# Optimization experiments

Hardware: AMD Instinct MI355X
Metric: run time of the kernel (lower is better)

## Reference

```python
import jax, jax.numpy as jnp
import numpy as np

H = 64  # hidden_dim
D = 16  # input_dim


def _gru_scan(x, w_ih, w_hh, b_ih, b_hh):
    """Single-direction GRU (PyTorch gate order r,z,n).
    x: [B,T,D] -> ys: [T,B,H] (hidden at each step), h_last: [B,H]."""
    B = x.shape[0]
    # precompute input-to-gate projections for all timesteps: [T,B,3H]
    xg = jnp.einsum('btd,gd->tbg', x, w_ih) + b_ih
    h0 = jnp.zeros((B, w_hh.shape[1]), dtype=x.dtype)

    def step(h, xg_t):
        hg = h @ w_hh.T + b_hh                      # [B,3H]
        xr, xz, xn = jnp.split(xg_t, 3, axis=-1)
        hr, hz, hn = jnp.split(hg, 3, axis=-1)
        r = jax.nn.sigmoid(xr + hr)
        z = jax.nn.sigmoid(xz + hz)
        n = jnp.tanh(xn + r * hn)
        h_new = (1.0 - z) * n + z * h
        return h_new, h_new

    h_last, ys = jax.lax.scan(step, h0, xg)
    return ys, h_last


def setup_inputs() -> dict:
    key = jax.random.key(0)
    ks = jax.random.split(key, 11)
    B, T = 512, 512
    s_i = 1.0 / np.sqrt(H)
    x = jax.random.normal(ks[0], (B, T, D), dtype=jnp.float32)
    def u(k, shape):
        return jax.random.uniform(k, shape, dtype=jnp.float32, minval=-s_i, maxval=s_i)
    return {
        'x': x,
        'w_ih_f': u(ks[1], (3 * H, D)), 'w_hh_f': u(ks[2], (3 * H, H)),
        'b_ih_f': u(ks[3], (3 * H,)),  'b_hh_f': u(ks[4], (3 * H,)),
        'w_ih_b': u(ks[5], (3 * H, D)), 'w_hh_b': u(ks[6], (3 * H, H)),
        'b_ih_b': u(ks[7], (3 * H,)),  'b_hh_b': u(ks[8], (3 * H,)),
        'fc_w': u(ks[9], (1, 2 * H)),  'fc_b': u(ks[10], (1,)),
    }


def reference(x, w_ih_f, w_hh_f, b_ih_f, b_hh_f,
              w_ih_b, w_hh_b, b_ih_b, b_hh_b, fc_w, fc_b):
    # forward direction: output at t=T-1 is the final carry
    _, h_fwd_last = _gru_scan(x, w_ih_f, w_hh_f, b_ih_f, b_hh_f)
    # backward direction: runs over reversed time; its output at original
    # t=T-1 is the FIRST step of the reversed scan
    ys_b, _ = _gru_scan(x[:, ::-1, :], w_ih_b, w_hh_b, b_ih_b, b_hh_b)
    h_bwd_at_last = ys_b[0]                          # [B,H]
    out_last = jnp.concatenate([h_fwd_last, h_bwd_at_last], axis=-1)  # [B,2H]
    y = out_last @ fc_w.T + fc_b                     # [B,1]
    return jnp.squeeze(y, axis=-1)                   # [B]
```

## Files before the change

### kernel.cpp

```cpp
#include <hip/hip_runtime.h>


#define Hh 64
#define Dd 16
#define Tt 512
#define Bb 512
#define CH 32
#define NC (Tt / CH)
#define PLANE (CH * Hh)
#define BUFSZ (3 * PLANE)

typedef float v2f __attribute__((ext_vector_type(2)));

__device__ __forceinline__ float rcp_fast(float v) { return __builtin_amdgcn_rcpf(v); }
__device__ __forceinline__ float sigmoid_fast(float v) {
    return rcp_fast(1.0f + __expf(-v));
}
__device__ __forceinline__ float tanh_fast(float v) {
    return 1.0f - 2.0f * rcp_fast(__expf(2.0f * v) + 1.0f);
}
__device__ __forceinline__ float dot4(float4 a, float4 b) {
    return a.x * b.x + a.y * b.y + a.z * b.z + a.w * b.w;
}
__device__ __forceinline__ void pkfma(v2f& a, v2f b, v2f c) {
    asm("v_pk_fma_f32 %0, %1, %2, %0" : "+v"(a) : "v"(b), "v"(c));
}
__device__ __forceinline__ void lds_barrier() {
    asm volatile("s_waitcnt lgkmcnt(0)\n\ts_barrier" ::: "memory");
}

#define QPK(Q, QI)                                                           \
    {                                                                        \
        const v2f lo_ = { Q.x, Q.y };                                        \
        const v2f hi_ = { Q.z, Q.w };                                        \
        pkfma(ar0, wr2[2*(QI)],     lo_);                                    \
        pkfma(az0, wz2[2*(QI)],     lo_);                                    \
        pkfma(an0, wn2[2*(QI)],     lo_);                                    \
        pkfma(ar1, wr2[2*(QI) + 1], hi_);                                    \
        pkfma(az1, wz2[2*(QI) + 1], hi_);                                    \
        pkfma(an1, wn2[2*(QI) + 1], hi_);                                    \
    }

__global__ __launch_bounds__(256, 2)
void bigru_pc_kernel(const float* __restrict__ x,
                     const float* __restrict__ w_ih_f, const float* __restrict__ w_hh_f,
                     const float* __restrict__ b_ih_f, const float* __restrict__ b_hh_f,
                     const float* __restrict__ w_ih_b, const float* __restrict__ w_hh_b,
                     const float* __restrict__ b_ih_b, const float* __restrict__ b_hh_b,
                     const float* __restrict__ fc_w,  const float* __restrict__ fc_b,
                     float* __restrict__ out)
{
    const int tid  = threadIdx.x;
    const int j    = tid & 63;
    const int w    = tid >> 6;
    const int b    = blockIdx.x;
    const int cons = b & 3;

    __shared__ __align__(16) float xgs[2 * BUFSZ];
    __shared__ __align__(16) float hbuf[Hh];

    const float* xrow = x + (size_t)b * Tt * Dd;

    if (w == cons) {
        v2f wr2[Hh/2], wz2[Hh/2], wn2[Hh/2];
        {
            const float4* r0 = (const float4*)(w_hh_f + (size_t)j            * Hh);
            const float4* r1 = (const float4*)(w_hh_f + (size_t)(Hh + j)     * Hh);
            const float4* r2 = (const float4*)(w_hh_f + (size_t)(2 * Hh + j) * Hh);
#pragma unroll
            for (int q = 0; q < Hh / 4; ++q) {
                float4 a = r0[q]; wr2[2*q] = (v2f){a.x, a.y}; wr2[2*q+1] = (v2f){a.z, a.w};
                float4 c = r1[q]; wz2[2*q] = (v2f){c.x, c.y}; wz2[2*q+1] = (v2f){c.z, c.w};
                float4 e = r2[q]; wn2[2*q] = (v2f){e.x, e.y}; wn2[2*q+1] = (v2f){e.z, e.w};
            }
        }
        const float bhnr = b_hh_f[2 * Hh + j];
        float h = 0.0f;

        for (int c = 0; c < NC; ++c) {
            lds_barrier();
            const float* base = xgs + (c & 1) * BUFSZ + j;
            float par = base[0];
            float paz = base[PLANE];
            float pan = base[2 * PLANE];
#pragma unroll 2
            for (int t = 0; t < CH; ++t) {
                hbuf[j] = h;
                const float4* hq = (const float4*)hbuf;
                float4 q0 = hq[0],  q1 = hq[1],  q2 = hq[2],  q3 = hq[3];
                float4 q4 = hq[4],  q5 = hq[5],  q6 = hq[6],  q7 = hq[7];
                const int tn = (t + 1) & (CH - 1);
                const float* p = base + tn * Hh;
                const float nar = p[0];
                const float naz = p[PLANE];
                const float nan = p[2 * PLANE];

                v2f ar0 = {0.f, 0.f}, ar1 = {0.f, 0.f};
                v2f az0 = {0.f, 0.f}, az1 = {0.f, 0.f};
                v2f an0 = {0.f, 0.f}, an1 = {0.f, 0.f};

                QPK(q0, 0)  QPK(q1, 1)  QPK(q2, 2)  QPK(q3, 3)
                q0 = hq[8];  q1 = hq[9];  q2 = hq[10]; q3 = hq[11];
                QPK(q4, 4)  QPK(q5, 5)  QPK(q6, 6)  QPK(q7, 7)
                q4 = hq[12]; q5 = hq[13]; q6 = hq[14]; q7 = hq[15];
                QPK(q0, 8)  QPK(q1, 9)  QPK(q2, 10) QPK(q3, 11)
                QPK(q4, 12) QPK(q5, 13) QPK(q6, 14) QPK(q7, 15)

                const float sr = (ar0.x + ar0.y) + (ar1.x + ar1.y);
                const float sz = (az0.x + az0.y) + (az1.x + az1.y);
                const float sn = (an0.x + an0.y) + (an1.x + an1.y);

                const float r = sigmoid_fast(par + sr);
                const float z = sigmoid_fast(paz + sz);
                const float n = tanh_fast(pan + r * (bhnr + sn));
                h = n + z * (h - n);
                par = nar; paz = naz; pan = nan;
            }
        }

        float ar   = b_ih_b[j]          + b_hh_b[j];
        float az   = b_ih_b[Hh + j]     + b_hh_b[Hh + j];
        float axn  = b_ih_b[2 * Hh + j];
        const float bhnb = b_hh_b[2 * Hh + j];
        {
            const float4* xl = (const float4*)(xrow + (size_t)(Tt - 1) * Dd);
            float4 xv0 = xl[0], xv1 = xl[1], xv2 = xl[2], xv3 = xl[3];
            const float4* q0 = (const float4*)(w_ih_b + (size_t)j            * Dd);
            const float4* q1 = (const float4*)(w_ih_b + (size_t)(Hh + j)     * Dd);
            const float4* q2 = (const float4*)(w_ih_b + (size_t)(2 * Hh + j) * Dd);
            ar  += dot4(q0[0], xv0) + dot4(q0[1], xv1) + dot4(q0[2], xv2) + dot4(q0[3], xv3);
            az  += dot4(q1[0], xv0) + dot4(q1[1], xv1) + dot4(q1[2], xv2) + dot4(q1[3], xv3);
            axn += dot4(q2[0], xv0) + dot4(q2[1], xv1) + dot4(q2[2], xv2) + dot4(q2[3], xv3);
        }
        const float rb = sigmoid_fast(ar);
        const float zb = sigmoid_fast(az);
        const float nb = tanh_fast(axn + rb * bhnb);
        const float hb = (1.0f - zb) * nb;

        float v = fc_w[j] * h + fc_w[Hh + j] * hb;
#pragma unroll
        for (int off = 32; off > 0; off >>= 1)
            v += __shfl_xor(v, off, 64);
        if (j == 0) out[b] = v + fc_b[0];
    } else {
        const int pw = (w > cons) ? (w - 1) : w;
        float4 wir[4], wiz[4], win[4];
        {
            const float4* p0 = (const float4*)(w_ih_f + (size_t)j            * Dd);
            const float4* p1 = (const float4*)(w_ih_f + (size_t)(Hh + j)     * Dd);
            const float4* p2 = (const float4*)(w_ih_f + (size_t)(2 * Hh + j) * Dd);
#pragma unroll
            for (int q = 0; q < 4; ++q) { wir[q] = p0[q]; wiz[q] = p1[q]; win[q] = p2[q]; }
        }
        const float bxr = b_ih_f[j]          + b_hh_f[j];
        const float bxz = b_ih_f[Hh + j]     + b_hh_f[Hh + j];
        const float bxn = b_ih_f[2 * Hh + j];

#define PRODUCE(C1) {                                                        \
            float* obase = xgs + ((C1) & 1) * BUFSZ + j;                     \
            for (int tt = pw; tt < CH; tt += 3) {                            \
                const float4* xq = (const float4*)(xrow + (size_t)((C1) * CH + tt) * Dd); \
                float4 x0 = xq[0], x1 = xq[1], x2 = xq[2], x3 = xq[3];       \
                float ar_ = bxr + dot4(wir[0],x0) + dot4(wir[1],x1)          \
                                + dot4(wir[2],x2) + dot4(wir[3],x3);         \
                float az_ = bxz + dot4(wiz[0],x0) + dot4(wiz[1],x1)          \
                                + dot4(wiz[2],x2) + dot4(wiz[3],x3);         \
                float an_ = bxn + dot4(win[0],x0) + dot4(win[1],x1)          \
                                + dot4(win[2],x2) + dot4(win[3],x3);         \
                float* o = obase + tt * Hh;                                  \
                o[0] = ar_; o[PLANE] = az_; o[2 * PLANE] = an_;              \
            }                                                                \
        }

        PRODUCE(0);
        for (int c = 0; c < NC; ++c) {
            lds_barrier();
            if (c + 1 < NC) PRODUCE(c + 1);
        }
#undef PRODUCE
    }
}

extern "C" void kernel_launch(void* const* d_in, const int* in_sizes, int n_in,
                              void* d_out, int out_size, void* d_ws, size_t ws_size,
                              hipStream_t stream) {
    const float* x      = (const float*)d_in[0];
    const float* w_ih_f = (const float*)d_in[1];
    const float* w_hh_f = (const float*)d_in[2];
    const float* b_ih_f = (const float*)d_in[3];
    const float* b_hh_f = (const float*)d_in[4];
    const float* w_ih_b = (const float*)d_in[5];
    const float* w_hh_b = (const float*)d_in[6];
    const float* b_ih_b = (const float*)d_in[7];
    const float* b_hh_b = (const float*)d_in[8];
    const float* fc_w   = (const float*)d_in[9];
    const float* fc_b   = (const float*)d_in[10];

    bigru_pc_kernel<<<dim3(Bb), dim3(256), 0, stream>>>(
        x, w_ih_f, w_hh_f, b_ih_f, b_hh_f,
        w_ih_b, w_hh_b, b_ih_b, b_hh_b, fc_w, fc_b,
        (float*)d_out);
}
```

Measured before the change: 287.2 us.

## Process two batch rows per block to interleave independent GRU recurrences

```diff
diff --git a/kernel.cpp b/kernel.cpp
--- a/kernel.cpp
+++ b/kernel.cpp
@@ -5,10 +5,12 @@
 #define Dd 16
 #define Tt 512
 #define Bb 512
-#define CH 32
+#define NBLK (Bb / 2)
+#define CH 16
 #define NC (Tt / CH)
 #define PLANE (CH * Hh)
-#define BUFSZ (3 * PLANE)
+#define BATCHSZ (3 * PLANE)
+#define BUFSZ (2 * BATCHSZ)
 
 typedef float v2f __attribute__((ext_vector_type(2)));
 
@@ -29,37 +31,42 @@
     asm volatile("s_waitcnt lgkmcnt(0)\n\ts_barrier" ::: "memory");
 }
 
-#define QPK(Q, QI)                                                           \
+#define PAIRQ(QI, QA, QB)                                                    \
     {                                                                        \
-        const v2f lo_ = { Q.x, Q.y };                                        \
-        const v2f hi_ = { Q.z, Q.w };                                        \
-        pkfma(ar0, wr2[2*(QI)],     lo_);                                    \
-        pkfma(az0, wz2[2*(QI)],     lo_);                                    \
-        pkfma(an0, wn2[2*(QI)],     lo_);                                    \
-        pkfma(ar1, wr2[2*(QI) + 1], hi_);                                    \
-        pkfma(az1, wz2[2*(QI) + 1], hi_);                                    \
-        pkfma(an1, wn2[2*(QI) + 1], hi_);                                    \
+        const v2f la_ = { QA.x, QA.y }, ha_ = { QA.z, QA.w };                \
+        const v2f lb_ = { QB.x, QB.y }, hb_ = { QB.z, QB.w };                \
+        pkfma(arA, wr2[2*(QI)],   la_);                                      \
+        pkfma(azA, wz2[2*(QI)],   la_);                                      \
+        pkfma(anA, wn2[2*(QI)],   la_);                                      \
+        pkfma(arB, wr2[2*(QI)],   lb_);                                      \
+        pkfma(azB, wz2[2*(QI)],   lb_);                                      \
+        pkfma(anB, wn2[2*(QI)],   lb_);                                      \
+        pkfma(arA, wr2[2*(QI)+1], ha_);                                      \
+        pkfma(azA, wz2[2*(QI)+1], ha_);                                      \
+        pkfma(anA, wn2[2*(QI)+1], ha_);                                      \
+        pkfma(arB, wr2[2*(QI)+1], hb_);                                      \
+        pkfma(azB, wz2[2*(QI)+1], hb_);                                      \
+        pkfma(anB, wn2[2*(QI)+1], hb_);                                      \
     }
 
-__global__ __launch_bounds__(256, 2)
-void bigru_pc_kernel(const float* __restrict__ x,
-                     const float* __restrict__ w_ih_f, const float* __restrict__ w_hh_f,
-                     const float* __restrict__ b_ih_f, const float* __restrict__ b_hh_f,
-                     const float* __restrict__ w_ih_b, const float* __restrict__ w_hh_b,
-                     const float* __restrict__ b_ih_b, const float* __restrict__ b_hh_b,
-                     const float* __restrict__ fc_w,  const float* __restrict__ fc_b,
-                     float* __restrict__ out)
+__global__ __launch_bounds__(256, 1)
+void bigru_pc2_kernel(const float* __restrict__ x,
+                      const float* __restrict__ w_ih_f, const float* __restrict__ w_hh_f,
+                      const float* __restrict__ b_ih_f, const float* __restrict__ b_hh_f,
+                      const float* __restrict__ w_ih_b, const float* __restrict__ w_hh_b,
+                      const float* __restrict__ b_ih_b, const float* __restrict__ b_hh_b,
+                      const float* __restrict__ fc_w,  const float* __restrict__ fc_b,
+                      float* __restrict__ out)
 {
     const int tid  = threadIdx.x;
     const int j    = tid & 63;
     const int w    = tid >> 6;
-    const int b    = blockIdx.x;
-    const int cons = b & 3;
+    const int bb   = blockIdx.x;
+    const int b0   = bb * 2;
+    const int cons = bb & 3;
 
     __shared__ __align__(16) float xgs[2 * BUFSZ];
-    __shared__ __align__(16) float hbuf[Hh];
-
-    const float* xrow = x + (size_t)b * Tt * Dd;
+    __shared__ __align__(16) float hbuf[2 * Hh];
 
     if (w == cons) {
         v2f wr2[Hh/2], wz2[Hh/2], wn2[Hh/2];
@@ -75,73 +82,91 @@
             }
         }
         const float bhnr = b_hh_f[2 * Hh + j];
-        float h = 0.0f;
+        float hA = 0.0f, hB = 0.0f;
 
         for (int c = 0; c < NC; ++c) {
             lds_barrier();
-            const float* base = xgs + (c & 1) * BUFSZ + j;
-            float par = base[0];
-            float paz = base[PLANE];
-            float pan = base[2 * PLANE];
-#pragma unroll 2
+            const float* baseA = xgs + (c & 1) * BUFSZ + j;
+            const float* baseB = baseA + BATCHSZ;
+            float parA = baseA[0], pazA = baseA[PLANE], panA = baseA[2 * PLANE];
+            float parB = baseB[0], pazB = baseB[PLANE], panB = baseB[2 * PLANE];
+
             for (int t = 0; t < CH; ++t) {
-                hbuf[j] = h;
-                const float4* hq = (const float4*)hbuf;
-                float4 q0 = hq[0],  q1 = hq[1],  q2 = hq[2],  q3 = hq[3];
-                float4 q4 = hq[4],  q5 = hq[5],  q6 = hq[6],  q7 = hq[7];
+                hbuf[j] = hA;
+                hbuf[Hh + j] = hB;
+                const float4* hqA = (const float4*)hbuf;
+                const float4* hqB = (const float4*)(hbuf + Hh);
+                float4 a0 = hqA[0], a1 = hqA[1], a2 = hqA[2], a3 = hqA[3];
+                float4 q0 = hqB[0], q1 = hqB[1], q2 = hqB[2], q3 = hqB[3];
                 const int tn = (t + 1) & (CH - 1);
-                const float* p = base + tn * Hh;
-                const float nar = p[0];
-                const float naz = p[PLANE];
-                const float nan = p[2 * PLANE];
-
-                v2f ar0 = {0.f, 0.f}, ar1 = {0.f, 0.f};
-                v2f az0 = {0.f, 0.f}, az1 = {0.f, 0.f};
-                v2f an0 = {0.f, 0.f}, an1 = {0.f, 0.f};
-
-                QPK(q0, 0)  QPK(q1, 1)  QPK(q2, 2)  QPK(q3, 3)
-                q0 = hq[8];  q1 = hq[9];  q2 = hq[10]; q3 = hq[11];
-                QPK(q4, 4)  QPK(q5, 5)  QPK(q6, 6)  QPK(q7, 7)
-                q4 = hq[12]; q5 = hq[13]; q6 = hq[14]; q7 = hq[15];
-                QPK(q0, 8)  QPK(q1, 9)  QPK(q2, 10) QPK(q3, 11)
-                QPK(q4, 12) QPK(q5, 13) QPK(q6, 14) QPK(q7, 15)
-
-                const float sr = (ar0.x + ar0.y) + (ar1.x + ar1.y);
-                const float sz = (az0.x + az0.y) + (az1.x + az1.y);
-                const float sn = (an0.x + an0.y) + (an1.x + an1.y);
-
-                const float r = sigmoid_fast(par + sr);
-                const float z = sigmoid_fast(paz + sz);
-                const float n = tanh_fast(pan + r * (bhnr + sn));
-                h = n + z * (h - n);
-                par = nar; paz = naz; pan = nan;
+                const float* pA = baseA + tn * Hh;
+                const float* pB = baseB + tn * Hh;
+                const float narA = pA[0], nazA = pA[PLANE], nanA = pA[2 * PLANE];
+                const float narB = pB[0], nazB = pB[PLANE], nanB = pB[2 * PLANE];
+
+                v2f arA = {0.f,0.f}, azA = {0.f,0.f}, anA = {0.f,0.f};
+                v2f arB = {0.f,0.f}, azB = {0.f,0.f}, anB = {0.f,0.f};
+
+                PAIRQ(0, a0, q0)  PAIRQ(1, a1, q1)
+                a0 = hqA[4]; q0 = hqB[4]; a1 = hqA[5]; q1 = hqB[5];
+                PAIRQ(2, a2, q2)  PAIRQ(3, a3, q3)
+                a2 = hqA[6]; q2 = hqB[6]; a3 = hqA[7]; q3 = hqB[7];
+                PAIRQ(4, a0, q0)  PAIRQ(5, a1, q1)
+                a0 = hqA[8]; q0 = hqB[8]; a1 = hqA[9]; q1 = hqB[9];
+                PAIRQ(6, a2, q2)  PAIRQ(7, a3, q3)
+                a2 = hqA[10]; q2 = hqB[10]; a3 = hqA[11]; q3 = hqB[11];
+                PAIRQ(8, a0, q0)  PAIRQ(9, a1, q1)
+                a0 = hqA[12]; q0 = hqB[12]; a1 = hqA[13]; q1 = hqB[13];
+                PAIRQ(10, a2, q2) PAIRQ(11, a3, q3)
+                a2 = hqA[14]; q2 = hqB[14]; a3 = hqA[15]; q3 = hqB[15];
+                PAIRQ(12, a0, q0) PAIRQ(13, a1, q1)
+                PAIRQ(14, a2, q2) PAIRQ(15, a3, q3)
+
+                const float srA = arA.x + arA.y, szA = azA.x + azA.y, snA = anA.x + anA.y;
+                const float srB = arB.x + arB.y, szB = azB.x + azB.y, snB = anB.x + anB.y;
+
+                const float rA = sigmoid_fast(parA + srA);
+                const float rB = sigmoid_fast(parB + srB);
+                const float zA = sigmoid_fast(pazA + szA);
+                const float zB = sigmoid_fast(pazB + szB);
+                const float nA = tanh_fast(panA + rA * (bhnr + snA));
+                const float nB = tanh_fast(panB + rB * (bhnr + snB));
+                hA = nA + zA * (hA - nA);
+                hB = nB + zB * (hB - nB);
+                parA = narA; pazA = nazA; panA = nanA;
+                parB = narB; pazB = nazB; panB = nanB;
             }
         }
 
-        float ar   = b_ih_b[j]          + b_hh_b[j];
-        float az   = b_ih_b[Hh + j]     + b_hh_b[Hh + j];
-        float axn  = b_ih_b[2 * Hh + j];
-        const float bhnb = b_hh_b[2 * Hh + j];
-        {
-            const float4* xl = (const float4*)(xrow + (size_t)(Tt - 1) * Dd);
-            float4 xv0 = xl[0], xv1 = xl[1], xv2 = xl[2], xv3 = xl[3];
-            const float4* q0 = (const float4*)(w_ih_b + (size_t)j            * Dd);
-            const float4* q1 = (const float4*)(w_ih_b + (size_t)(Hh + j)     * Dd);
-            const float4* q2 = (const float4*)(w_ih_b + (size_t)(2 * Hh + j) * Dd);
-            ar  += dot4(q0[0], xv0) + dot4(q0[1], xv1) + dot4(q0[2], xv2) + dot4(q0[3], xv3);
-            az  += dot4(q1[0], xv0) + dot4(q1[1], xv1) + dot4(q1[2], xv2) + dot4(q1[3], xv3);
-            axn += dot4(q2[0], xv0) + dot4(q2[1], xv1) + dot4(q2[2], xv2) + dot4(q2[3], xv3);
-        }
-        const float rb = sigmoid_fast(ar);
-        const float zb = sigmoid_fast(az);
-        const float nb = tanh_fast(axn + rb * bhnb);
-        const float hb = (1.0f - zb) * nb;
-
-        float v = fc_w[j] * h + fc_w[Hh + j] * hb;
-#pragma unroll
-        for (int off = 32; off > 0; off >>= 1)
-            v += __shfl_xor(v, off, 64);
-        if (j == 0) out[b] = v + fc_b[0];
+#pragma unroll
+        for (int bi = 0; bi < 2; ++bi) {
+            const float hf = (bi == 0) ? hA : hB;
+            const float* xrow = x + (size_t)(b0 + bi) * Tt * Dd;
+            float ar   = b_ih_b[j]          + b_hh_b[j];
+            float az   = b_ih_b[Hh + j]     + b_hh_b[Hh + j];
+            float axn  = b_ih_b[2 * Hh + j];
+            const float bhnb = b_hh_b[2 * Hh + j];
+            {
+                const float4* xl = (const float4*)(xrow + (size_t)(Tt - 1) * Dd);
+                float4 xv0 = xl[0], xv1 = xl[1], xv2 = xl[2], xv3 = xl[3];
+                const float4* q0 = (const float4*)(w_ih_b + (size_t)j            * Dd);
+                const float4* q1 = (const float4*)(w_ih_b + (size_t)(Hh + j)     * Dd);
+                const float4* q2 = (const float4*)(w_ih_b + (size_t)(2 * Hh + j) * Dd);
+                ar  += dot4(q0[0], xv0) + dot4(q0[1], xv1) + dot4(q0[2], xv2) + dot4(q0[3], xv3);
+                az  += dot4(q1[0], xv0) + dot4(q1[1], xv1) + dot4(q1[2], xv2) + dot4(q1[3], xv3);
+                axn += dot4(q2[0], xv0) + dot4(q2[1], xv1) + dot4(q2[2], xv2) + dot4(q2[3], xv3);
+            }
+            const float rb = sigmoid_fast(ar);
+            const float zb = sigmoid_fast(az);
+            const float nb = tanh_fast(axn + rb * bhnb);
+            const float hb = (1.0f - zb) * nb;
+
+            float v = fc_w[j] * hf + fc_w[Hh + j] * hb;
+#pragma unroll
+            for (int off = 32; off > 0; off >>= 1)
+                v += __shfl_xor(v, off, 64);
+            if (j == 0) out[b0 + bi] = v + fc_b[0];
+        }
     } else {
         const int pw = (w > cons) ? (w - 1) : w;
         float4 wir[4], wiz[4], win[4];
@@ -158,8 +183,11 @@
 
 #define PRODUCE(C1) {                                                        \
             float* obase = xgs + ((C1) & 1) * BUFSZ + j;                     \
-            for (int tt = pw; tt < CH; tt += 3) {                            \
-                const float4* xq = (const float4*)(xrow + (size_t)((C1) * CH + tt) * Dd); \
+            for (int idx = pw; idx < 2 * CH; idx += 3) {                     \
+                const int bi = idx / CH;                                     \
+                const int tt = idx - bi * CH;                                \
+                const float4* xq = (const float4*)(x +                       \
+                    ((size_t)(b0 + bi) * Tt + (size_t)(C1) * CH + tt) * Dd); \
                 float4 x0 = xq[0], x1 = xq[1], x2 = xq[2], x3 = xq[3];       \
                 float ar_ = bxr + dot4(wir[0],x0) + dot4(wir[1],x1)          \
                                 + dot4(wir[2],x2) + dot4(wir[3],x3);         \
@@ -167,7 +195,7 @@
                                 + dot4(wiz[2],x2) + dot4(wiz[3],x3);         \
                 float an_ = bxn + dot4(win[0],x0) + dot4(win[1],x1)          \
                                 + dot4(win[2],x2) + dot4(win[3],x3);         \
-                float* o = obase + tt * Hh;                                  \
+                float* o = obase + bi * BATCHSZ + tt * Hh;                   \
                 o[0] = ar_; o[PLANE] = az_; o[2 * PLANE] = an_;              \
             }                                                                \
         }
@@ -196,7 +224,7 @@
     const float* fc_w   = (const float*)d_in[9];
     const float* fc_b   = (const float*)d_in[10];
 
-    bigru_pc_kernel<<<dim3(Bb), dim3(256), 0, stream>>>(
+    bigru_pc2_kernel<<<dim3(NBLK), dim3(256), 0, stream>>>(
         x, w_ih_f, w_hh_f, b_ih_f, b_hh_f,
         w_ih_b, w_hh_b, b_ih_b, b_hh_b, fc_w, fc_b,
         (float*)d_out);
```

New measurement: 421.8 us. 46.9% more time.

## Pack gate preactivations into float4 LDS entries and halve chunk size

Applied to the files above, without the earlier changes.

```diff
diff --git a/kernel.cpp b/kernel.cpp
--- a/kernel.cpp
+++ b/kernel.cpp
@@ -5,10 +5,9 @@
 #define Dd 16
 #define Tt 512
 #define Bb 512
-#define CH 32
+#define CH 16
 #define NC (Tt / CH)
-#define PLANE (CH * Hh)
-#define BUFSZ (3 * PLANE)
+#define BUFSZ (CH * Hh)
 
 typedef float v2f __attribute__((ext_vector_type(2)));
 
@@ -56,8 +55,8 @@
     const int b    = blockIdx.x;
     const int cons = b & 3;
 
-    __shared__ __align__(16) float xgs[2 * BUFSZ];
-    __shared__ __align__(16) float hbuf[Hh];
+    __shared__ __align__(16) float4 xgs4[2 * BUFSZ];
+    __shared__ __align__(16) float  hbuf[Hh];
 
     const float* xrow = x + (size_t)b * Tt * Dd;
 
@@ -79,25 +78,19 @@
 
         for (int c = 0; c < NC; ++c) {
             lds_barrier();
-            const float* base = xgs + (c & 1) * BUFSZ + j;
-            float par = base[0];
-            float paz = base[PLANE];
-            float pan = base[2 * PLANE];
+            const float4* base = xgs4 + (c & 1) * BUFSZ + j;
+            float4 pg = base[0];
 #pragma unroll 2
             for (int t = 0; t < CH; ++t) {
+                float4 ng = base[((t + 1) & (CH - 1)) * Hh];
                 hbuf[j] = h;
                 const float4* hq = (const float4*)hbuf;
                 float4 q0 = hq[0],  q1 = hq[1],  q2 = hq[2],  q3 = hq[3];
                 float4 q4 = hq[4],  q5 = hq[5],  q6 = hq[6],  q7 = hq[7];
-                const int tn = (t + 1) & (CH - 1);
-                const float* p = base + tn * Hh;
-                const float nar = p[0];
-                const float naz = p[PLANE];
-                const float nan = p[2 * PLANE];
 
-                v2f ar0 = {0.f, 0.f}, ar1 = {0.f, 0.f};
-                v2f az0 = {0.f, 0.f}, az1 = {0.f, 0.f};
-                v2f an0 = {0.f, 0.f}, an1 = {0.f, 0.f};
+                v2f ar0 = {0.f,0.f}, ar1 = {0.f,0.f};
+                v2f az0 = {0.f,0.f}, az1 = {0.f,0.f};
+                v2f an0 = {0.f,0.f}, an1 = {0.f,0.f};
 
                 QPK(q0, 0)  QPK(q1, 1)  QPK(q2, 2)  QPK(q3, 3)
                 q0 = hq[8];  q1 = hq[9];  q2 = hq[10]; q3 = hq[11];
@@ -110,11 +103,11 @@
                 const float sz = (az0.x + az0.y) + (az1.x + az1.y);
                 const float sn = (an0.x + an0.y) + (an1.x + an1.y);
 
-                const float r = sigmoid_fast(par + sr);
-                const float z = sigmoid_fast(paz + sz);
-                const float n = tanh_fast(pan + r * (bhnr + sn));
+                const float r = sigmoid_fast(pg.x + sr);
+                const float z = sigmoid_fast(pg.y + sz);
+                const float n = tanh_fast(pg.z + r * (bhnr + sn));
                 h = n + z * (h - n);
-                par = nar; paz = naz; pan = nan;
+                pg = ng;
             }
         }
 
@@ -157,7 +150,7 @@
         const float bxn = b_ih_f[2 * Hh + j];
 
 #define PRODUCE(C1) {                                                        \
-            float* obase = xgs + ((C1) & 1) * BUFSZ + j;                     \
+            float4* obase = xgs4 + ((C1) & 1) * BUFSZ + j;                   \
             for (int tt = pw; tt < CH; tt += 3) {                            \
                 const float4* xq = (const float4*)(xrow + (size_t)((C1) * CH + tt) * Dd); \
                 float4 x0 = xq[0], x1 = xq[1], x2 = xq[2], x3 = xq[3];       \
@@ -167,8 +160,7 @@
                                 + dot4(wiz[2],x2) + dot4(wiz[3],x3);         \
                 float an_ = bxn + dot4(win[0],x0) + dot4(win[1],x1)          \
                                 + dot4(win[2],x2) + dot4(win[3],x3);         \
-                float* o = obase + tt * Hh;                                  \
-                o[0] = ar_; o[PLANE] = az_; o[2 * PLANE] = an_;              \
+                obase[tt * Hh] = make_float4(ar_, az_, an_, 0.0f);           \
             }                                                                \
         }
 
```

Measured after the change: 291.7 us. No clear change (+1.6%).
